# Kernel optimization log

Measured on AMD Instinct MI355X. Metric: run time of the kernel, lower is better.

## Reference

```python
import jax, jax.numpy as jnp
import numpy as np

B, L, D = 2, 2048, 1024
NUM_HEADS = 16
HEAD_DIM = D // NUM_HEADS


def setup_inputs() -> dict:
    key = jax.random.key(0)
    k1, k2 = jax.random.split(key)
    x = jax.random.normal(k1, (B, L, D), dtype=jnp.float32)
    # torch Linear(input_dim, 3*output_dim, bias=False); store as [in, 3*out] for x @ W
    W_qkv = jax.random.normal(k2, (D, 3 * D), dtype=jnp.float32) * (1.0 / np.sqrt(D))
    return {"x": x, "W_qkv": W_qkv}


def reference(x, W_qkv):
    b, l, d = x.shape
    h, hd = NUM_HEADS, HEAD_DIM
    qkv = x @ W_qkv                                  # [B, L, 3*D]
    qkv = qkv.reshape(b, l, 3, h, hd)
    q = jnp.transpose(qkv[:, :, 0], (0, 2, 1, 3))    # [B, H, L, hd]
    k = jnp.transpose(qkv[:, :, 1], (0, 2, 1, 3))
    v = jnp.transpose(qkv[:, :, 2], (0, 2, 1, 3))
    scale = 1.0 / jnp.sqrt(jnp.asarray(hd, dtype=x.dtype))
    scores = jnp.einsum('bhqd,bhkd->bhqk', q, k) * scale   # [B, H, L, L]
    causal = jnp.triu(jnp.ones((l, l), dtype=bool), k=1)   # True above diagonal -> masked
    scores = jnp.where(causal, -jnp.inf, scores)
    attn = jax.nn.softmax(scores, axis=-1)
    # dropout p=0.0 -> identity (eval mode)
    out = jnp.einsum('bhqk,bhkd->bhqd', attn, v)            # [B, H, L, hd]
    out = jnp.transpose(out, (0, 2, 1, 3)).reshape(b, l, h * hd)
    return out
```

## Files before the change

kernel.cpp:

```cpp
#include <hip/hip_runtime.h>
#include <hip/hip_bf16.h>
#include <math.h>

#define NB_L 2048
#define GM 4096
#define GN 3072
#define GK 1024
#define NROWS 65536
#define SCALE_L2E 0.180336880f

typedef float  f4v __attribute__((ext_vector_type(4)));
typedef short  s4v __attribute__((ext_vector_type(4)));
typedef short  s8v __attribute__((ext_vector_type(8)));

#define MFMA_16x16x32(a, b, c) __builtin_amdgcn_mfma_f32_16x16x32_bf16((a), (b), (c), 0, 0, 0)
#define MFMA_16x16x16(a, b, c) __builtin_amdgcn_mfma_f32_16x16x16bf16_1k((a), (b), (c), 0, 0, 0)

static __device__ __forceinline__ unsigned int bfpk(float a, float b) {
    __hip_bfloat162 h = __float22bfloat162_rn(float2{a, b});
    union { __hip_bfloat162 h2; unsigned int u; } cv; cv.h2 = h; return cv.u;
}
static __device__ __forceinline__ unsigned int pkrnd(float a, float b) {
    union { float f; unsigned int u; } ua, ub;
    ua.f = a; ub.f = b;
    return __builtin_amdgcn_perm(ub.u + 0x8000u, ua.u + 0x8000u, 0x07060302u);
}
static __device__ __forceinline__ unsigned short bf1(float a) {
    union { __hip_bfloat16 h; unsigned short u; } cv; cv.h = __float2bfloat16(a); return cv.u;
}
static __device__ __forceinline__ float bf2f(unsigned short u) {
    union { unsigned int u; float f; } cv; cv.u = ((unsigned int)u) << 16; return cv.f;
}

static __device__ __forceinline__ void gl_lds16(const ushort* g, ushort* l) {
    __builtin_amdgcn_global_load_lds((const __attribute__((address_space(1))) void*)g,
                                     (__attribute__((address_space(3))) void*)l, 16, 0, 0);
}

__global__ __launch_bounds__(256) void conv_fused(
    const float* __restrict__ X, const float* __restrict__ W,
    ushort* __restrict__ Xb, ushort* __restrict__ Wt)
{
    __shared__ __align__(16) ushort T[64][72];
    const int bid = blockIdx.x, t = threadIdx.x;
    if (bid < 2048) {
        const int i = bid * 256 + t;
        const float4 f0 = ((const float4*)X)[2 * i];
        const float4 f1 = ((const float4*)X)[2 * i + 1];
        uint4 u;
        u.x = bfpk(f0.x, f0.y); u.y = bfpk(f0.z, f0.w);
        u.z = bfpk(f1.x, f1.y); u.w = bfpk(f1.z, f1.w);
        ((uint4*)Xb)[i] = u;
    } else {
        const int wb = bid - 2048;
        const int k0 = (wb & 15) * 64, n0 = (wb >> 4) * 64;
        {
            const int kr = t >> 2, nc0 = (t & 3) * 16;
            const float* src = W + (size_t)(k0 + kr) * GN + n0 + nc0;
#pragma unroll
            for (int u = 0; u < 4; ++u) {
                const float4 v = *(const float4*)(src + 4 * u);
                T[nc0 + 4 * u + 0][kr] = bf1(v.x);
                T[nc0 + 4 * u + 1][kr] = bf1(v.y);
                T[nc0 + 4 * u + 2][kr] = bf1(v.z);
                T[nc0 + 4 * u + 3][kr] = bf1(v.w);
            }
        }
        __syncthreads();
        {
            const int nr = t >> 2, kc0 = (t & 3) * 16;
            ushort* dst = Wt + (size_t)(n0 + nr) * GK + k0 + kc0;
            *(s8v*)dst       = *(const s8v*)&T[nr][kc0];
            *(s8v*)(dst + 8) = *(const s8v*)&T[nr][kc0 + 8];
        }
    }
}

__global__ __launch_bounds__(512, 2) void qkv_gemm_bf16(
    const ushort* __restrict__ Xb, const ushort* __restrict__ Wt,
    ushort* __restrict__ Qh, ushort* __restrict__ Kh, ushort* __restrict__ VT)
{
    __shared__ __align__(16) ushort As[2][2][128][32];
    __shared__ __align__(16) ushort Bs[2][2][384][32];

    const int tid = threadIdx.x;
    const int bid = blockIdx.x;

    const int xcd = bid & 7, idx = bid >> 3;
    const int ytile = ((xcd >> 1) << 3) + (idx & 7);
    const int xtile = ((xcd & 1) << 2) + (idx >> 3);
    const int row0 = ytile << 7;
    const int col0 = xtile * 384;

    const int lane = tid & 63, w = tid >> 6;
    const int wm = w >> 2, wn = w & 3;
    const int lq = lane & 15, quad = lane >> 4;

    const int rS = tid >> 2, pA = tid & 3;
    const int cA = pA ^ ((rS >> 1) & 3);
    const ushort* gA0 = Xb + (size_t)(row0 + rS) * GK + cA * 8;
    const ushort* gB0 = Wt + (size_t)(col0 + rS) * GK + cA * 8;

    const int pq = (quad ^ ((lq >> 1) & 3)) * 8;
    const int rowA = wm * 64 + lq;
    const int rowB = wn * 96 + lq;

    f4v acc[4][6];
#pragma unroll
    for (int mf = 0; mf < 4; ++mf)
#pragma unroll
        for (int nf = 0; nf < 6; ++nf) acc[mf][nf] = 0.f;

    auto stA = [&](int t, int h) {
        gl_lds16(gA0 + t * 64 + h * 32, &As[t & 1][h][rS][pA * 8]);
    };
    auto stB = [&](int t, int h, int u) {
        gl_lds16(gB0 + (size_t)u * 128 * GK + t * 64 + h * 32,
                 &Bs[t & 1][h][u * 128 + rS][pA * 8]);
    };

    stA(0, 0);
    stB(0, 0, 0); stB(0, 0, 1); stB(0, 0, 2);
    stA(0, 1);
    stB(0, 1, 0); stB(0, 1, 1); stB(0, 1, 2);
    stA(1, 0);
    stB(1, 0, 0); stB(1, 0, 1); stB(1, 0, 2);
    asm volatile("s_waitcnt vmcnt(4)" ::: "memory");
    __builtin_amdgcn_s_barrier();
    asm volatile("" ::: "memory");

    const int NT = GK / 64;
#pragma unroll 2
    for (int t = 0; t < NT; ++t) {
        const int cur = t & 1;
        s8v af[4], bfr[3];

#pragma unroll
        for (int nf = 0; nf < 3; ++nf) bfr[nf] = *(const s8v*)&Bs[cur][0][rowB + nf * 16][pq];
#pragma unroll
        for (int mf = 0; mf < 4; ++mf) af[mf] = *(const s8v*)&As[cur][0][rowA + mf * 16][pq];
        if (t + 1 < NT) { stB(t + 1, 1, 0); stB(t + 1, 1, 1); stB(t + 1, 1, 2); }
        __builtin_amdgcn_s_barrier();
        asm volatile("s_waitcnt lgkmcnt(0)");
        __builtin_amdgcn_s_setprio(1);
#pragma unroll
        for (int mf = 0; mf < 4; ++mf)
#pragma unroll
            for (int nf = 0; nf < 3; ++nf)
                acc[mf][nf] = MFMA_16x16x32(af[mf], bfr[nf], acc[mf][nf]);
        __builtin_amdgcn_s_setprio(0);
        __builtin_amdgcn_s_barrier();

#pragma unroll
        for (int nf = 0; nf < 3; ++nf) bfr[nf] = *(const s8v*)&Bs[cur][0][rowB + 48 + nf * 16][pq];
        if (t + 1 < NT) stA(t + 1, 1);
        __builtin_amdgcn_s_barrier();
        asm volatile("s_waitcnt lgkmcnt(0)");
        __builtin_amdgcn_s_setprio(1);
#pragma unroll
        for (int mf = 0; mf < 4; ++mf)
#pragma unroll
            for (int nf = 0; nf < 3; ++nf)
                acc[mf][nf + 3] = MFMA_16x16x32(af[mf], bfr[nf], acc[mf][nf + 3]);
        __builtin_amdgcn_s_setprio(0);
        __builtin_amdgcn_s_barrier();

#pragma unroll
        for (int nf = 0; nf < 3; ++nf) bfr[nf] = *(const s8v*)&Bs[cur][1][rowB + nf * 16][pq];
#pragma unroll
        for (int mf = 0; mf < 4; ++mf) af[mf] = *(const s8v*)&As[cur][1][rowA + mf * 16][pq];
        if (t + 2 < NT) stA(t + 2, 0);
        __builtin_amdgcn_s_barrier();
        asm volatile("s_waitcnt lgkmcnt(0)");
        __builtin_amdgcn_s_setprio(1);
#pragma unroll
        for (int mf = 0; mf < 4; ++mf)
#pragma unroll
            for (int nf = 0; nf < 3; ++nf)
                acc[mf][nf] = MFMA_16x16x32(af[mf], bfr[nf], acc[mf][nf]);
        __builtin_amdgcn_s_setprio(0);
        __builtin_amdgcn_s_barrier();

#pragma unroll
        for (int nf = 0; nf < 3; ++nf) bfr[nf] = *(const s8v*)&Bs[cur][1][rowB + 48 + nf * 16][pq];
        if (t + 2 < NT) { stB(t + 2, 0, 0); stB(t + 2, 0, 1); stB(t + 2, 0, 2); }
        __builtin_amdgcn_s_barrier();
        asm volatile("s_waitcnt lgkmcnt(0)");
        __builtin_amdgcn_s_setprio(1);
#pragma unroll
        for (int mf = 0; mf < 4; ++mf)
#pragma unroll
            for (int nf = 0; nf < 3; ++nf)
                acc[mf][nf + 3] = MFMA_16x16x32(af[mf], bfr[nf], acc[mf][nf + 3]);
        __builtin_amdgcn_s_setprio(0);
        if (t + 2 < NT) asm volatile("s_waitcnt vmcnt(4)" ::: "memory");
        else            asm volatile("s_waitcnt vmcnt(0)" ::: "memory");
        __builtin_amdgcn_s_barrier();
        asm volatile("" ::: "memory");
    }

#pragma unroll
    for (int mf = 0; mf < 4; ++mf)
#pragma unroll
        for (int nf = 0; nf < 6; ++nf) {
            const int colg = col0 + wn * 96 + nf * 16 + lq;
            const int part = colg >> 10;
            const int colp = colg & 1023;
            const int hh = colp >> 6, d = colp & 63;
#pragma unroll
            for (int r = 0; r < 4; ++r) {
                const int row = row0 + wm * 64 + mf * 16 + quad * 4 + r;
                const int b = row >> 11, tok = row & 2047;
                const int bh = b * 16 + hh;
                if (part == 0) {
                    Qh[((size_t)bh * 2048 + tok) * 64 + d] = bf1(acc[mf][nf][r] * SCALE_L2E);
                } else if (part == 1) {
                    Kh[((size_t)bh * 2048 + tok) * 64 + (d ^ ((tok & 7) << 3))] = bf1(acc[mf][nf][r]);
                } else {
                    VT[((size_t)bh * 64 + d) * 2048 + (tok ^ ((d & 7) << 3))] = bf1(acc[mf][nf][r]);
                }
            }
        }
}

__global__ __launch_bounds__(256, 4) void attn_bf16(
    const ushort* __restrict__ Qh, const ushort* __restrict__ Kh,
    const ushort* __restrict__ VT, ushort* __restrict__ Opart, float* __restrict__ Lp)
{
    __shared__ __align__(16) ushort Ks[2][64 * 64];
    __shared__ __align__(16) ushort Vt[2][64 * 64];

    const int x = blockIdx.x;
    const int bh = x & 31;
    const int y = x >> 5;
    const int s = y & 1;
    const int qp = y >> 1;

    const int tid = threadIdx.x;
    const int w = tid >> 6, lane = tid & 63;
    const int lq = lane & 15, quad = lane >> 4;
    const int kswz = (lq & 7) << 3;

    const ushort* kbase = Kh + (size_t)bh * 2048 * 64;
    const ushort* vbase = VT + (size_t)bh * 64 * 2048;
    const int g1 = tid, g2 = tid + 256;
    const int kr1 = g1 >> 3, ko1 = (g1 & 7) * 8;
    const int kr2 = g2 >> 3, ko2 = (g2 & 7) * 8;

    auto stage = [&](int kt, int bufi) {
        const ushort* kt_k = kbase + (size_t)kt * 64 * 64;
        const ushort* kt_v = vbase + kt * 64;
        gl_lds16(kt_k + kr1 * 64 + ko1,           &Ks[bufi][g1 * 8]);
        gl_lds16(kt_k + kr2 * 64 + ko2,           &Ks[bufi][g2 * 8]);
        gl_lds16(kt_v + (size_t)kr1 * 2048 + ko1, &Vt[bufi][g1 * 8]);
        gl_lds16(kt_v + (size_t)kr2 * 2048 + ko2, &Vt[bufi][g2 * 8]);
    };

    const s4v ones = { (short)0x3F80, (short)0x3F80, (short)0x3F80, (short)0x3F80 };

#pragma unroll 1
    for (int piece = 0; piece < 2; ++piece) {
        const int qt = piece ? (15 - qp) : qp;
        const int qrow_base = qt * 128 + w * 32;
        const int diag = 2 * qt + (w >> 1);
        const int kt_lo = s ? (qt + 1) : 0;
        const int niter = qt + 1;

        if (piece) __builtin_amdgcn_s_barrier();

        s8v qf[2][2];
#pragma unroll
        for (int qg = 0; qg < 2; ++qg)
#pragma unroll
            for (int sb = 0; sb < 2; ++sb)
                qf[qg][sb] = *(const s8v*)(Qh + ((size_t)bh * 2048 + qrow_base + qg * 16 + lq) * 64
                                           + sb * 32 + quad * 8);

        f4v o[4][2];
#pragma unroll
        for (int dg = 0; dg < 4; ++dg)
#pragma unroll
            for (int qg = 0; qg < 2; ++qg) o[dg][qg] = 0.f;
        f4v lacc[2]; lacc[0] = 0.f; lacc[1] = 0.f;

        auto compute = [&](int ktc, int bufi) {
            if (ktc > diag) return;
            f4v st[4][2];
#pragma unroll
            for (int kg = 0; kg < 4; ++kg)
#pragma unroll
                for (int qg = 0; qg < 2; ++qg) st[kg][qg] = 0.f;
#pragma unroll
            for (int kg = 0; kg < 4; ++kg)
#pragma unroll
                for (int sb = 0; sb < 2; ++sb) {
                    const s8v af = *(const s8v*)&Ks[bufi][(kg * 16 + lq) * 64
                                                         + ((sb * 32 + quad * 8) ^ kswz)];
#pragma unroll
                    for (int qg = 0; qg < 2; ++qg)
                        st[kg][qg] = MFMA_16x16x32(af, qf[qg][sb], st[kg][qg]);
                }
            if (ktc == diag) {
#pragma unroll
                for (int kg = 0; kg < 4; ++kg)
#pragma unroll
                    for (int qg = 0; qg < 2; ++qg) {
                        const int qrow = qrow_base + qg * 16 + lq;
#pragma unroll
                        for (int r = 0; r < 4; ++r)
                            if (ktc * 64 + kg * 16 + quad * 4 + r > qrow)
                                st[kg][qg][r] = -INFINITY;
                    }
            }
#pragma unroll
            for (int kg = 0; kg < 4; ++kg)
#pragma unroll
                for (int qg = 0; qg < 2; ++qg)
#pragma unroll
                    for (int r = 0; r < 4; ++r)
                        st[kg][qg][r] = exp2f(st[kg][qg][r]);
#pragma unroll
            for (int ks = 0; ks < 4; ++ks) {
                s4v pb[2];
#pragma unroll
                for (int qg = 0; qg < 2; ++qg) {
                    union { s4v v; uint2 u; } c;
                    c.u.x = pkrnd(st[ks][qg][0], st[ks][qg][1]);
                    c.u.y = pkrnd(st[ks][qg][2], st[ks][qg][3]);
                    pb[qg] = c.v;
                }
#pragma unroll
                for (int qg = 0; qg < 2; ++qg)
                    lacc[qg] = MFMA_16x16x16(ones, pb[qg], lacc[qg]);
#pragma unroll
                for (int dg = 0; dg < 4; ++dg) {
                    const s4v va = *(const s4v*)&Vt[bufi][(dg * 16 + lq) * 64
                                                         + ((ks * 16 + quad * 4) ^ kswz)];
#pragma unroll
                    for (int qg = 0; qg < 2; ++qg)
                        o[dg][qg] = MFMA_16x16x16(va, pb[qg], o[dg][qg]);
                }
            }
        };

        stage(kt_lo, 0);
#pragma unroll 1
        for (int i = 0; i < niter; ++i) {
            const int cur = i & 1;
            __builtin_amdgcn_s_barrier();
            if (i + 1 < niter) {
                stage(kt_lo + i + 1, cur ^ 1);
                asm volatile("s_waitcnt vmcnt(4)" ::: "memory");
            } else {
                asm volatile("s_waitcnt vmcnt(0)" ::: "memory");
            }
            __builtin_amdgcn_s_barrier();
            compute(kt_lo + i, cur);
        }

#pragma unroll
        for (int qg = 0; qg < 2; ++qg) {
            const size_t prow = (size_t)(s * 32 + bh) * 2048 + qrow_base + qg * 16 + lq;
#pragma unroll
            for (int dg = 0; dg < 4; ++dg) {
                const int d = dg * 16 + quad * 4;
                uint2 u;
                u.x = bfpk(o[dg][qg][0], o[dg][qg][1]);
                u.y = bfpk(o[dg][qg][2], o[dg][qg][3]);
                *(uint2*)&Opart[prow * 64 + d] = u;
            }
            if (quad == 0) Lp[prow] = lacc[qg][0];
        }
    }
}

__global__ __launch_bounds__(256) void attn_combine(
    const ushort* __restrict__ Opart, const float* __restrict__ Lp, float* __restrict__ Out)
{
    const int id = blockIdx.x * 256 + threadIdx.x;
    const int row = id >> 4, c4 = (id & 15) * 4;
    const float l0 = Lp[row], l1 = Lp[row + NROWS];
    const float inv = 1.0f / (l0 + l1);

    const s4v a = *(const s4v*)&Opart[(size_t)row * 64 + c4];
    const s4v c = *(const s4v*)&Opart[(size_t)(row + NROWS) * 64 + c4];
    float4 v;
    v.x = (bf2f((unsigned short)a[0]) + bf2f((unsigned short)c[0])) * inv;
    v.y = (bf2f((unsigned short)a[1]) + bf2f((unsigned short)c[1])) * inv;
    v.z = (bf2f((unsigned short)a[2]) + bf2f((unsigned short)c[2])) * inv;
    v.w = (bf2f((unsigned short)a[3]) + bf2f((unsigned short)c[3])) * inv;

    const int bh = row >> 11, qrow = row & 2047;
    const int b = bh >> 4, h = bh & 15;
    *(float4*)(Out + ((size_t)(b * 2048 + qrow)) * 1024 + h * 64 + c4) = v;
}

extern "C" void kernel_launch(void* const* d_in, const int* in_sizes, int n_in,
                              void* d_out, int out_size, void* d_ws, size_t ws_size,
                              hipStream_t stream)
{
    const float* x  = (const float*)d_in[0];
    const float* wq = (const float*)d_in[1];
    float* out = (float*)d_out;

    const size_t HEADTEN = (size_t)32 * 2048 * 64;
    ushort* wsp = (ushort*)d_ws;
    ushort* qh = wsp;
    ushort* kh = qh + HEADTEN;
    ushort* vt = kh + HEADTEN;
    ushort* xb = vt + HEADTEN;
    ushort* wt = xb + (size_t)GM * GK;
    ushort* opart = xb;
    float*  lp    = (float*)(opart + (size_t)2 * NROWS * 64);

    conv_fused<<<2816, 256, 0, stream>>>(x, wq, xb, wt);
    qkv_gemm_bf16<<<256, 512, 0, stream>>>(xb, wt, qh, kh, vt);
    attn_bf16<<<512, 256, 0, stream>>>(qh, kh, vt, opart, lp);
    attn_combine<<<NROWS * 16 / 256, 256, 0, stream>>>(opart, lp, out);
}
```

Before: 171.6 us.

## Use 8 waves per attention block with 16 query rows each

The attention kernel moves from 4 waves of 32 query rows to 8 waves of 16 query rows per block, launching 512 threads. Each thread now issues one K and one V global-to-LDS load per stage, and the wait count drops to match. This halves per-wave accumulator registers and raises wave-level parallelism, which should improve latency hiding. In exchange, each K/V fragment read from LDS feeds only one MFMA instead of two, doubling LDS read traffic per unit of compute, and barriers now synchronise more waves.

```diff
diff --git a/kernel.cpp b/kernel.cpp
--- a/kernel.cpp
+++ b/kernel.cpp
@@ -223,7 +223,7 @@
         }
 }
 
-__global__ __launch_bounds__(256, 4) void attn_bf16(
+__global__ __launch_bounds__(512, 4) void attn_bf16(
     const ushort* __restrict__ Qh, const ushort* __restrict__ Kh,
     const ushort* __restrict__ VT, ushort* __restrict__ Opart, float* __restrict__ Lp)
 {
@@ -243,17 +243,11 @@
 
     const ushort* kbase = Kh + (size_t)bh * 2048 * 64;
     const ushort* vbase = VT + (size_t)bh * 64 * 2048;
-    const int g1 = tid, g2 = tid + 256;
-    const int kr1 = g1 >> 3, ko1 = (g1 & 7) * 8;
-    const int kr2 = g2 >> 3, ko2 = (g2 & 7) * 8;
+    const int kr = tid >> 3, ko = (tid & 7) * 8;
 
     auto stage = [&](int kt, int bufi) {
-        const ushort* kt_k = kbase + (size_t)kt * 64 * 64;
-        const ushort* kt_v = vbase + kt * 64;
-        gl_lds16(kt_k + kr1 * 64 + ko1,           &Ks[bufi][g1 * 8]);
-        gl_lds16(kt_k + kr2 * 64 + ko2,           &Ks[bufi][g2 * 8]);
-        gl_lds16(kt_v + (size_t)kr1 * 2048 + ko1, &Vt[bufi][g1 * 8]);
-        gl_lds16(kt_v + (size_t)kr2 * 2048 + ko2, &Vt[bufi][g2 * 8]);
+        gl_lds16(kbase + (size_t)kt * 64 * 64 + kr * 64 + ko, &Ks[bufi][tid * 8]);
+        gl_lds16(vbase + (size_t)kr * 2048 + kt * 64 + ko,    &Vt[bufi][tid * 8]);
     };
 
     const s4v ones = { (short)0x3F80, (short)0x3F80, (short)0x3F80, (short)0x3F80 };
@@ -261,84 +255,66 @@
 #pragma unroll 1
     for (int piece = 0; piece < 2; ++piece) {
         const int qt = piece ? (15 - qp) : qp;
-        const int qrow_base = qt * 128 + w * 32;
-        const int diag = 2 * qt + (w >> 1);
+        const int qrow_base = qt * 128 + w * 16;
+        const int diag = 2 * qt + (w >> 2);
         const int kt_lo = s ? (qt + 1) : 0;
         const int niter = qt + 1;
 
         if (piece) __builtin_amdgcn_s_barrier();
 
-        s8v qf[2][2];
-#pragma unroll
-        for (int qg = 0; qg < 2; ++qg)
-#pragma unroll
-            for (int sb = 0; sb < 2; ++sb)
-                qf[qg][sb] = *(const s8v*)(Qh + ((size_t)bh * 2048 + qrow_base + qg * 16 + lq) * 64
-                                           + sb * 32 + quad * 8);
-
-        f4v o[4][2];
-#pragma unroll
-        for (int dg = 0; dg < 4; ++dg)
-#pragma unroll
-            for (int qg = 0; qg < 2; ++qg) o[dg][qg] = 0.f;
-        f4v lacc[2]; lacc[0] = 0.f; lacc[1] = 0.f;
+        s8v qf[2];
+#pragma unroll
+        for (int sb = 0; sb < 2; ++sb)
+            qf[sb] = *(const s8v*)(Qh + ((size_t)bh * 2048 + qrow_base + lq) * 64
+                                   + sb * 32 + quad * 8);
+
+        f4v o[4];
+#pragma unroll
+        for (int dg = 0; dg < 4; ++dg) o[dg] = 0.f;
+        f4v lacc = 0.f;
 
         auto compute = [&](int ktc, int bufi) {
             if (ktc > diag) return;
-            f4v st[4][2];
-#pragma unroll
-            for (int kg = 0; kg < 4; ++kg)
-#pragma unroll
-                for (int qg = 0; qg < 2; ++qg) st[kg][qg] = 0.f;
+            f4v st[4];
+#pragma unroll
+            for (int kg = 0; kg < 4; ++kg) st[kg] = 0.f;
 #pragma unroll
             for (int kg = 0; kg < 4; ++kg)
 #pragma unroll
                 for (int sb = 0; sb < 2; ++sb) {
                     const s8v af = *(const s8v*)&Ks[bufi][(kg * 16 + lq) * 64
                                                          + ((sb * 32 + quad * 8) ^ kswz)];
-#pragma unroll
-                    for (int qg = 0; qg < 2; ++qg)
-                        st[kg][qg] = MFMA_16x16x32(af, qf[qg][sb], st[kg][qg]);
+                    st[kg] = MFMA_16x16x32(af, qf[sb], st[kg]);
                 }
             if (ktc == diag) {
+                const int qrow = qrow_base + lq;
 #pragma unroll
                 for (int kg = 0; kg < 4; ++kg)
 #pragma unroll
-                    for (int qg = 0; qg < 2; ++qg) {
-                        const int qrow = qrow_base + qg * 16 + lq;
-#pragma unroll
-                        for (int r = 0; r < 4; ++r)
-                            if (ktc * 64 + kg * 16 + quad * 4 + r > qrow)
-                                st[kg][qg][r] = -INFINITY;
-                    }
+                    for (int r = 0; r < 4; ++r)
+                        if (ktc * 64 + kg * 16 + quad * 4 + r > qrow)
+                            st[kg][r] = -INFINITY;
             }
 #pragma unroll
             for (int kg = 0; kg < 4; ++kg)
 #pragma unroll
-                for (int qg = 0; qg < 2; ++qg)
-#pragma unroll
-                    for (int r = 0; r < 4; ++r)
-                        st[kg][qg][r] = exp2f(st[kg][qg][r]);
+                for (int r = 0; r < 4; ++r)
+                    st[kg][r] = exp2f(st[kg][r]);
 #pragma unroll
             for (int ks = 0; ks < 4; ++ks) {
-                s4v pb[2];
-#pragma unroll
-                for (int qg = 0; qg < 2; ++qg) {
+                s4v pb;
+                {
                     union { s4v v; uint2 u; } c;
-                    c.u.x = pkrnd(st[ks][qg][0], st[ks][qg][1]);
-                    c.u.y = pkrnd(st[ks][qg][2], st[ks][qg][3]);
-                    pb[qg] = c.v;
+                    c.u.x = pkrnd(st[ks][0], st[ks][1]);
+                    c.u.y = pkrnd(st[ks][2], st[ks][3]);
+                    pb = c.v;
                 }
-#pragma unroll
-                for (int qg = 0; qg < 2; ++qg)
-                    lacc[qg] = MFMA_16x16x16(ones, pb[qg], lacc[qg]);
+                lacc = MFMA_16x16x16(ones, pb, lacc);
 #pragma unroll
                 for (int dg = 0; dg < 4; ++dg) {
                     const s4v va = *(const s4v*)&Vt[bufi][(dg * 16 + lq) * 64
                                                          + ((ks * 16 + quad * 4) ^ kswz)];
-#pragma unroll
-                    for (int qg = 0; qg < 2; ++qg)
-                        o[dg][qg] = MFMA_16x16x16(va, pb[qg], o[dg][qg]);
+                    o[dg] = MFMA_16x16x16(va, pb, o[dg]);
                 }
             }
         };
@@ -350,7 +326,7 @@
             __builtin_amdgcn_s_barrier();
             if (i + 1 < niter) {
                 stage(kt_lo + i + 1, cur ^ 1);
-                asm volatile("s_waitcnt vmcnt(4)" ::: "memory");
+                asm volatile("s_waitcnt vmcnt(2)" ::: "memory");
             } else {
                 asm volatile("s_waitcnt vmcnt(0)" ::: "memory");
             }
@@ -358,18 +334,17 @@
             compute(kt_lo + i, cur);
         }
 
-#pragma unroll
-        for (int qg = 0; qg < 2; ++qg) {
-            const size_t prow = (size_t)(s * 32 + bh) * 2048 + qrow_base + qg * 16 + lq;
+        {
+            const size_t prow = (size_t)(s * 32 + bh) * 2048 + qrow_base + lq;
 #pragma unroll
             for (int dg = 0; dg < 4; ++dg) {
                 const int d = dg * 16 + quad * 4;
                 uint2 u;
-                u.x = bfpk(o[dg][qg][0], o[dg][qg][1]);
-                u.y = bfpk(o[dg][qg][2], o[dg][qg][3]);
+                u.x = bfpk(o[dg][0], o[dg][1]);
+                u.y = bfpk(o[dg][2], o[dg][3]);
                 *(uint2*)&Opart[prow * 64 + d] = u;
             }
-            if (quad == 0) Lp[prow] = lacc[qg][0];
+            if (quad == 0) Lp[prow] = lacc[0];
         }
     }
 }
@@ -415,6 +390,6 @@
 
     conv_fused<<<2816, 256, 0, stream>>>(x, wq, xb, wt);
     qkv_gemm_bf16<<<256, 512, 0, stream>>>(xb, wt, qh, kh, vt);
-    attn_bf16<<<512, 256, 0, stream>>>(qh, kh, vt, opart, lp);
+    attn_bf16<<<512, 512, 0, stream>>>(qh, kh, vt, opart, lp);
     attn_combine<<<NROWS * 16 / 256, 256, 0, stream>>>(opart, lp, out);
 }
```

Result: faster. 163.9 us (median of 2 runs) (-4.5%).
